# Kernel optimization log

Hardware: AMD Instinct MI355X
Metric: run time of the kernel (lower is better)

## Reference

```python
import jax, jax.numpy as jnp
import numpy as np

B, T, D, H = 4, 2048, 1024, 16
HD = D // H  # head_size = 64
EPS = 1e-5


def layernorm(x, g, b):
    mu = jnp.mean(x, axis=-1, keepdims=True)
    var = jnp.var(x, axis=-1, keepdims=True)
    return (x - mu) * jax.lax.rsqrt(var + EPS) * g + b


def setup_inputs() -> dict:
    key = jax.random.key(0)
    ks = jax.random.split(key, 8)
    s = 0.02
    return {
        "x": jax.random.normal(ks[0], (B, T, D), jnp.float32),
        "Wq": jax.random.normal(ks[1], (D, D), jnp.float32) * s,
        "Wk": jax.random.normal(ks[2], (D, D), jnp.float32) * s,
        "Wv": jax.random.normal(ks[3], (D, D), jnp.float32) * s,
        "Wo": jax.random.normal(ks[4], (D, D), jnp.float32) * s,
        "bo": jnp.zeros((D,), jnp.float32),
        "W1": jax.random.normal(ks[5], (D, 4 * D), jnp.float32) * s,
        "b1": jnp.zeros((4 * D,), jnp.float32),
        "W2": jax.random.normal(ks[6], (4 * D, D), jnp.float32) * s,
        "b2": jnp.zeros((D,), jnp.float32),
        "ln1_g": jnp.ones((D,), jnp.float32),
        "ln1_b": jnp.zeros((D,), jnp.float32),
        "ln2_g": jnp.ones((D,), jnp.float32),
        "ln2_b": jnp.zeros((D,), jnp.float32),
    }


def reference(x, Wq, Wk, Wv, Wo, bo, W1, b1, W2, b2, ln1_g, ln1_b, ln2_g, ln2_b):
    # --- multi-head causal self-attention (pre-LN), dropout off (eval) ---
    h = layernorm(x, ln1_g, ln1_b)
    q = jnp.einsum('btd,de->bte', h, Wq).reshape(B, T, H, HD)
    k = jnp.einsum('btd,de->bte', h, Wk).reshape(B, T, H, HD)
    v = jnp.einsum('btd,de->bte', h, Wv).reshape(B, T, H, HD)
    scores = jnp.einsum('bqhd,bkhd->bhqk', q, k) * (HD ** -0.5)
    causal = jnp.tril(jnp.ones((T, T), bool))
    scores = jnp.where(causal, scores, -jnp.inf)
    attn = jax.nn.softmax(scores, axis=-1)
    out = jnp.einsum('bhqk,bkhd->bqhd', attn, v).reshape(B, T, D)
    out = jnp.einsum('btd,de->bte', out, Wo) + bo
    x = x + out
    # --- feed-forward: Linear -> ReLU -> Linear -> ReLU (as in source) ---
    h2 = layernorm(x, ln2_g, ln2_b)
    ff = jax.nn.relu(jnp.einsum('btd,df->btf', h2, W1) + b1)
    ff = jax.nn.relu(jnp.einsum('btf,fd->btd', ff, W2) + b2)
    return x + ff
```

## Files before the change

### kernel.cpp

```cpp
#include <hip/hip_runtime.h>
#include <cstdint>
#include <cstddef>

typedef unsigned short u16;
typedef __attribute__((ext_vector_type(8))) short bf16x8;
typedef __attribute__((ext_vector_type(4))) float f32x4;
typedef __attribute__((address_space(1))) const unsigned int gu32;
typedef __attribute__((address_space(3))) unsigned int lu32;

#define QSCALE 0.1803368801111204f

__device__ __forceinline__ u16 f2bf(float f) {
  uint32_t u = __float_as_uint(f);
  u += 0x7fffu + ((u >> 16) & 1u);
  return (u16)(u >> 16);
}

__global__ __launch_bounds__(256) void transpose_w(const float* __restrict__ W,
                                                   u16* __restrict__ WT,
                                                   int K, int N) {
  __shared__ float t[32][33];
  int n0 = blockIdx.x * 32, k0 = blockIdx.y * 32;
  for (int i = threadIdx.y; i < 32; i += 8)
    t[i][threadIdx.x] = W[(size_t)(k0 + i) * N + n0 + threadIdx.x];
  __syncthreads();
  for (int i = threadIdx.y; i < 32; i += 8)
    WT[(size_t)(n0 + i) * K + k0 + threadIdx.x] = f2bf(t[threadIdx.x][i]);
}

__global__ __launch_bounds__(256) void ln_kernel(const float* __restrict__ x,
                                                 const float* __restrict__ g,
                                                 const float* __restrict__ b,
                                                 u16* __restrict__ out) {
  int row = blockIdx.x;
  const float4 v = *(const float4*)(x + (size_t)row * 1024 + threadIdx.x * 4);
  float s = v.x + v.y + v.z + v.w;
  float ss = v.x * v.x + v.y * v.y + v.z * v.z + v.w * v.w;
#pragma unroll
  for (int d = 1; d < 64; d <<= 1) { s += __shfl_xor(s, d); ss += __shfl_xor(ss, d); }
  __shared__ float rs_[4], rss_[4];
  int wv = threadIdx.x >> 6;
  if ((threadIdx.x & 63) == 0) { rs_[wv] = s; rss_[wv] = ss; }
  __syncthreads();
  s = rs_[0] + rs_[1] + rs_[2] + rs_[3];
  ss = rss_[0] + rss_[1] + rss_[2] + rss_[3];
  float mu = s * (1.f / 1024.f);
  float var = ss * (1.f / 1024.f) - mu * mu;
  float rstd = rsqrtf(var + 1e-5f);
  float4 gv = *(const float4*)(g + threadIdx.x * 4);
  float4 bv = *(const float4*)(b + threadIdx.x * 4);
  uint32_t lo = (uint32_t)f2bf((v.x - mu) * rstd * gv.x + bv.x) |
                ((uint32_t)f2bf((v.y - mu) * rstd * gv.y + bv.y) << 16);
  uint32_t hi = (uint32_t)f2bf((v.z - mu) * rstd * gv.z + bv.z) |
                ((uint32_t)f2bf((v.w - mu) * rstd * gv.w + bv.w) << 16);
  uint2 o; o.x = lo; o.y = hi;
  *(uint2*)(out + (size_t)row * 1024 + threadIdx.x * 4) = o;
}

#define STAGEA(slot, tnext, is)                                               \
  __builtin_amdgcn_global_load_lds(                                           \
      (gu32*)((const char*)(A + (size_t)(bm * 256 + (is) * 64 + srow) * K +   \
                            (size_t)(tnext) * 64) + ssw),                     \
      (lu32*)&lds[(slot) * 24576 + (is) * 4096 + wid * 512], 16, 0, 0)
#define STAGEB(slot, tnext, is)                                               \
  __builtin_amdgcn_global_load_lds(                                           \
      (gu32*)((const char*)(BT + (size_t)(bn * 128 + (is) * 64 + srow) * K +  \
                            (size_t)(tnext) * 64) + ssw),                     \
      (lu32*)&lds[(slot) * 24576 + 16384 + (is) * 4096 + wid * 512], 16, 0, 0)

template <int MODE>
__global__ __launch_bounds__(512, 2) void gemm8p(
    const u16* __restrict__ A, const u16* __restrict__ BT,
    int M, int N, int K,
    const float* __restrict__ bias, const float* __restrict__ resid,
    float* __restrict__ outf,
    u16* __restrict__ ob0, u16* __restrict__ ob1, u16* __restrict__ ob2) {
  __shared__ __align__(16) u16 lds[73728];
  const int tid = threadIdx.x, lane = tid & 63, wid = tid >> 6;
  const int wr = wid >> 1, wc = wid & 1;
  const int bm = blockIdx.y, bn = blockIdx.x;
  const int l15 = lane & 15, lhi = lane >> 4;
  const int srow = tid >> 3;
  const int ssw = ((tid & 7) * 16) ^ ((srow & 7) << 4);
  const int cs0 = (lhi * 8) ^ ((l15 & 7) << 3);
  const int cs1 = (32 + lhi * 8) ^ ((l15 & 7) << 3);
  const int arow = (wr * 64 + l15) * 64;
  const int brow = (wc * 64 + l15) * 64;

  f32x4 acc[4][4];
#pragma unroll
  for (int i = 0; i < 4; ++i)
#pragma unroll
    for (int j = 0; j < 4; ++j) acc[i][j] = (f32x4){0.f, 0.f, 0.f, 0.f};

  const int NT = K >> 6;

#pragma unroll
  for (int t0 = 0; t0 < 2; ++t0) {
    STAGEA(t0, t0, 0); STAGEA(t0, t0, 1); STAGEA(t0, t0, 2); STAGEA(t0, t0, 3);
    STAGEB(t0, t0, 0); STAGEB(t0, t0, 1);
  }
  asm volatile("s_waitcnt vmcnt(6)" ::: "memory");
  __builtin_amdgcn_s_barrier();

  int s = 0, sn = 2;
  for (int t = 0; t < NT; ++t) {
    const bool hasPre = (t + 2) < NT;
    const int aoff = s * 24576, boff = s * 24576 + 16384;

    bf16x8 bfr[4][2], afr[2][2];
#pragma unroll
    for (int ni = 0; ni < 4; ++ni) {
      bfr[ni][0] = *(const bf16x8*)&lds[boff + brow + ni * 1024 + cs0];
      bfr[ni][1] = *(const bf16x8*)&lds[boff + brow + ni * 1024 + cs1];
    }
    afr[0][0] = *(const bf16x8*)&lds[aoff + arow + cs0];
    afr[0][1] = *(const bf16x8*)&lds[aoff + arow + cs1];
    afr[1][0] = *(const bf16x8*)&lds[aoff + arow + 1024 + cs0];
    afr[1][1] = *(const bf16x8*)&lds[aoff + arow + 1024 + cs1];
    if (hasPre) { STAGEA(sn, t + 2, 0); STAGEA(sn, t + 2, 1); STAGEB(sn, t + 2, 0); }
    __builtin_amdgcn_s_barrier();
    __builtin_amdgcn_s_setprio(1);
#pragma unroll
    for (int ks = 0; ks < 2; ++ks)
#pragma unroll
      for (int ml = 0; ml < 2; ++ml)
#pragma unroll
        for (int ni = 0; ni < 4; ++ni)
          acc[ml][ni] = __builtin_amdgcn_mfma_f32_16x16x32_bf16(afr[ml][ks], bfr[ni][ks], acc[ml][ni], 0, 0, 0);
    __builtin_amdgcn_s_setprio(0);
    __builtin_amdgcn_s_barrier();

    afr[0][0] = *(const bf16x8*)&lds[aoff + arow + 2048 + cs0];
    afr[0][1] = *(const bf16x8*)&lds[aoff + arow + 2048 + cs1];
    afr[1][0] = *(const bf16x8*)&lds[aoff + arow + 3072 + cs0];
    afr[1][1] = *(const bf16x8*)&lds[aoff + arow + 3072 + cs1];
    if (hasPre) { STAGEA(sn, t + 2, 2); STAGEA(sn, t + 2, 3); STAGEB(sn, t + 2, 1); }
    __builtin_amdgcn_s_barrier();
    __builtin_amdgcn_s_setprio(1);
#pragma unroll
    for (int ks = 0; ks < 2; ++ks)
#pragma unroll
      for (int ml = 0; ml < 2; ++ml)
#pragma unroll
        for (int ni = 0; ni < 4; ++ni)
          acc[2 + ml][ni] = __builtin_amdgcn_mfma_f32_16x16x32_bf16(afr[ml][ks], bfr[ni][ks], acc[2 + ml][ni], 0, 0, 0);
    __builtin_amdgcn_s_setprio(0);
    if (hasPre) {
      asm volatile("s_waitcnt vmcnt(6)" ::: "memory");
    } else if (t + 1 < NT) {
      asm volatile("s_waitcnt vmcnt(0)" ::: "memory");
    }
    __builtin_amdgcn_s_barrier();

    s = (s == 2) ? 0 : s + 1;
    sn = (sn == 2) ? 0 : sn + 1;
  }

#pragma unroll
  for (int mi = 0; mi < 4; ++mi) {
#pragma unroll
    for (int ni = 0; ni < 4; ++ni) {
      int col = bn * 128 + wc * 64 + ni * 16 + l15;
      int rbase = bm * 256 + wr * 64 + mi * 16 + lhi * 4;
#pragma unroll
      for (int r = 0; r < 4; ++r) {
        float v = acc[mi][ni][r];
        int rg = rbase + r;
        if (MODE == 0) {
          int b = rg >> 11, tt = rg & 2047;
          int cm = col & 1023, h = cm >> 6, d = cm & 63;
          size_t bh = (size_t)(b * 16 + h);
          if (col < 1024)
            ob0[(bh * 2048 + tt) * 64 + d] = f2bf(v * QSCALE);
          else if (col < 2048)
            ob1[(bh * 2048 + tt) * 64 + d] = f2bf(v);
          else
            ob2[(bh * 64 + d) * 2048 + tt] = f2bf(v);
        } else if (MODE == 1) {
          outf[(size_t)rg * N + col] = v + bias[col] + resid[(size_t)rg * N + col];
        } else if (MODE == 2) {
          ob0[(size_t)rg * N + col] = f2bf(fmaxf(v + bias[col], 0.f));
        } else {
          outf[(size_t)rg * N + col] = fmaxf(v + bias[col], 0.f) + resid[(size_t)rg * N + col];
        }
      }
    }
  }
}

__global__ __launch_bounds__(512) void attn_kernel(
    const u16* __restrict__ Qb, const u16* __restrict__ Kb,
    const u16* __restrict__ VTb, u16* __restrict__ O) {
  const int p = blockIdx.x;
  const int bh = blockIdx.y;
  const u16* Q = Qb + (size_t)bh * 2048 * 64;
  const u16* Kp = Kb + (size_t)bh * 2048 * 64;
  const u16* VT = VTb + (size_t)bh * 64 * 2048;
  const int tid = threadIdx.x, lane = tid & 63, wv = tid >> 6;
  const int l15 = lane & 15, lhi = lane >> 4;
  const int srow = tid >> 3;
  const int scol16 = (tid & 7) * 16;
  const int sw = scol16 ^ ((srow & 7) << 4);
  const int rswz = (l15 & 7) << 4;
  const int cb0 = (lhi * 16) ^ rswz;
  const int cb1 = (64 + lhi * 16) ^ rswz;
  const int b = bh >> 4, h = bh & 15;

  __shared__ __align__(16) u16 KV[2][2][4096];
  __shared__ u16 Ps[8][16 * 72];

#define STAGEKV(slot, kt)                                                     \
  do {                                                                        \
    __builtin_amdgcn_global_load_lds(                                         \
        (gu32*)((const char*)(Kp + (size_t)((kt)*64 + srow) * 64) + sw),      \
        (lu32*)&KV[slot][0][wv * 512], 16, 0, 0);                             \
    __builtin_amdgcn_global_load_lds(                                         \
        (gu32*)((const char*)(VT + (size_t)srow * 2048 + (kt)*64) + sw),      \
        (lu32*)&KV[slot][1][wv * 512], 16, 0, 0);                             \
  } while (0)

#pragma unroll
  for (int pass = 0; pass < 2; ++pass) {
    const int chunk = pass ? p : (15 - p);
    const int qbase = chunk * 128 + wv * 16;
    const int nkt = 2 * chunk + 2;

    bf16x8 qf[2];
#pragma unroll
    for (int ks = 0; ks < 2; ++ks)
      qf[ks] = *(const bf16x8*)&Q[(size_t)(qbase + l15) * 64 + ks * 32 + lhi * 8];

    f32x4 o[4];
#pragma unroll
    for (int f = 0; f < 4; ++f) o[f] = (f32x4){0.f, 0.f, 0.f, 0.f};
    float m = -1e30f;
    float l = 0.f;

    __syncthreads();
    STAGEKV(0, 0);

    for (int kt = 0; kt < nkt; ++kt) {
      const int cs = kt & 1;
      asm volatile("s_waitcnt vmcnt(0)" ::: "memory");
      __syncthreads();
      if (kt + 1 < nkt) STAGEKV(cs ^ 1, kt + 1);

      if (kt * 64 <= qbase + 15) {
        const char* Kbase = (const char*)&KV[cs][0][0];
        const char* Vbase = (const char*)&KV[cs][1][0];

        f32x4 s[4];
#pragma unroll
        for (int jt = 0; jt < 4; ++jt) s[jt] = (f32x4){0.f, 0.f, 0.f, 0.f};
        __builtin_amdgcn_s_setprio(1);
#pragma unroll
        for (int ks = 0; ks < 2; ++ks) {
          const int cbyte = ks ? cb1 : cb0;
#pragma unroll
          for (int jt = 0; jt < 4; ++jt) {
            bf16x8 kf = *(const bf16x8*)(Kbase + (jt * 16 + l15) * 128 + cbyte);
            s[jt] = __builtin_amdgcn_mfma_f32_16x16x32_bf16(kf, qf[ks], s[jt], 0, 0, 0);
          }
        }
        __builtin_amdgcn_s_setprio(0);

        if (kt * 64 + 63 > qbase) {
          int qg = qbase + l15;
#pragma unroll
          for (int jt = 0; jt < 4; ++jt)
#pragma unroll
            for (int r = 0; r < 4; ++r) {
              int kg = kt * 64 + jt * 16 + lhi * 4 + r;
              if (kg > qg) s[jt][r] = -1e30f;
            }
        }

        float mr = fmaxf(fmaxf(s[0][0], s[0][1]), fmaxf(s[0][2], s[0][3]));
#pragma unroll
        for (int jt = 1; jt < 4; ++jt)
          mr = fmaxf(mr, fmaxf(fmaxf(s[jt][0], s[jt][1]), fmaxf(s[jt][2], s[jt][3])));
        mr = fmaxf(mr, __shfl_xor(mr, 16));
        mr = fmaxf(mr, __shfl_xor(mr, 32));
        if (__any(mr > m + 8.f)) {
          float mn = fmaxf(m, mr);
          float sc = exp2f(m - mn);
          l *= sc;
          m = mn;
#pragma unroll
          for (int r = 0; r < 4; ++r) {
            float so = __shfl(sc, lhi * 4 + r);
#pragma unroll
            for (int f = 0; f < 4; ++f) o[f][r] *= so;
          }
        }

        float rs = 0.f;
#pragma unroll
        for (int jt = 0; jt < 4; ++jt)
#pragma unroll
          for (int r = 0; r < 4; ++r) {
            float pv = exp2f(s[jt][r] - m);
            s[jt][r] = pv;
            rs += pv;
          }
        rs += __shfl_xor(rs, 16);
        rs += __shfl_xor(rs, 32);
        l += rs;

#pragma unroll
        for (int jt = 0; jt < 4; ++jt) {
          uint32_t lo, hi;
          asm("v_cvt_pk_bf16_f32 %0, %1, %2"
              : "=v"(lo) : "v"(s[jt][0]), "v"(s[jt][1]));
          asm("v_cvt_pk_bf16_f32 %0, %1, %2"
              : "=v"(hi) : "v"(s[jt][2]), "v"(s[jt][3]));
          uint2 pk; pk.x = lo; pk.y = hi;
          *(uint2*)&Ps[wv][l15 * 72 + jt * 16 + lhi * 4] = pk;
        }
        __builtin_amdgcn_s_setprio(1);
#pragma unroll
        for (int ks = 0; ks < 2; ++ks) {
          const int cbyte = ks ? cb1 : cb0;
          bf16x8 pf = *(const bf16x8*)&Ps[wv][l15 * 72 + ks * 32 + lhi * 8];
#pragma unroll
          for (int f = 0; f < 4; ++f) {
            bf16x8 vfr = *(const bf16x8*)(Vbase + (f * 16 + l15) * 128 + cbyte);
            o[f] = __builtin_amdgcn_mfma_f32_16x16x32_bf16(pf, vfr, o[f], 0, 0, 0);
          }
        }
        __builtin_amdgcn_s_setprio(0);
      }
    }

#pragma unroll
    for (int r = 0; r < 4; ++r) {
      float ld = __shfl(l, lhi * 4 + r);
      float inv = 1.f / ld;
      int t = qbase + lhi * 4 + r;
#pragma unroll
      for (int f = 0; f < 4; ++f)
        O[((size_t)(b * 2048 + t)) * 1024 + h * 64 + f * 16 + l15] = f2bf(o[f][r] * inv);
    }
  }
#undef STAGEKV
}

extern "C" void kernel_launch(void* const* d_in, const int* in_sizes, int n_in,
                              void* d_out, int out_size, void* d_ws, size_t ws_size,
                              hipStream_t stream) {
  const float* x   = (const float*)d_in[0];
  const float* Wq  = (const float*)d_in[1];
  const float* Wk  = (const float*)d_in[2];
  const float* Wv  = (const float*)d_in[3];
  const float* Wo  = (const float*)d_in[4];
  const float* bo  = (const float*)d_in[5];
  const float* W1  = (const float*)d_in[6];
  const float* b1  = (const float*)d_in[7];
  const float* W2  = (const float*)d_in[8];
  const float* b2  = (const float*)d_in[9];
  const float* g1  = (const float*)d_in[10];
  const float* be1 = (const float*)d_in[11];
  const float* g2  = (const float*)d_in[12];
  const float* be2 = (const float*)d_in[13];

  char* p = (char*)d_ws;
  auto alloc = [&](size_t bytes) {
    char* r = p;
    p += (bytes + 255) & ~(size_t)255;
    return r;
  };
  u16* WqkvT = (u16*)alloc(3072ull * 1024 * 2);
  u16* WoT   = (u16*)alloc(1024ull * 1024 * 2);
  u16* W1T   = (u16*)alloc(4096ull * 1024 * 2);
  u16* W2T   = (u16*)alloc(1024ull * 4096 * 2);
  u16* hln   = (u16*)alloc(8192ull * 1024 * 2);
  u16* Qbuf  = (u16*)alloc(8192ull * 1024 * 2);
  u16* Kbuf  = (u16*)alloc(8192ull * 1024 * 2);
  u16* VTbuf = (u16*)alloc(8192ull * 1024 * 2);
  float* x2  = (float*)alloc(8192ull * 1024 * 4);
  u16* ff1   = (u16*)alloc(8192ull * 4096 * 2);
  u16* Oattn = hln;
  u16* h2    = Qbuf;
  if ((size_t)(p - (char*)d_ws) > ws_size) return;

  dim3 tb(32, 8);
  transpose_w<<<dim3(32, 32), tb, 0, stream>>>(Wq, WqkvT, 1024, 1024);
  transpose_w<<<dim3(32, 32), tb, 0, stream>>>(Wk, WqkvT + 1024 * 1024, 1024, 1024);
  transpose_w<<<dim3(32, 32), tb, 0, stream>>>(Wv, WqkvT + 2048 * 1024, 1024, 1024);
  transpose_w<<<dim3(32, 32), tb, 0, stream>>>(Wo, WoT, 1024, 1024);
  transpose_w<<<dim3(128, 32), tb, 0, stream>>>(W1, W1T, 1024, 4096);
  transpose_w<<<dim3(32, 128), tb, 0, stream>>>(W2, W2T, 4096, 1024);

  ln_kernel<<<8192, 256, 0, stream>>>(x, g1, be1, hln);

  gemm8p<0><<<dim3(24, 32), 512, 0, stream>>>(hln, WqkvT, 8192, 3072, 1024,
                                              nullptr, nullptr, nullptr,
                                              Qbuf, Kbuf, VTbuf);

  attn_kernel<<<dim3(8, 64), 512, 0, stream>>>(Qbuf, Kbuf, VTbuf, Oattn);

  gemm8p<1><<<dim3(8, 32), 512, 0, stream>>>(Oattn, WoT, 8192, 1024, 1024,
                                             bo, x, x2, nullptr, nullptr, nullptr);

  ln_kernel<<<8192, 256, 0, stream>>>(x2, g2, be2, h2);

  gemm8p<2><<<dim3(32, 32), 512, 0, stream>>>(h2, W1T, 8192, 4096, 1024,
                                              b1, nullptr, nullptr, ff1, nullptr, nullptr);

  gemm8p<3><<<dim3(8, 32), 512, 0, stream>>>(ff1, W2T, 8192, 1024, 4096,
                                             b2, x2, (float*)d_out, nullptr, nullptr, nullptr);
}
```

Baseline: 432.2 us.

## Stage GEMM epilogue through LDS for coalesced vector stores; keep Q/K row-major

The bf16-output GEMM epilogues (QKV projection and FFN1) now write the converted accumulators into shared memory first, then emit 16-byte coalesced global stores. The V^T tile is transposed through LDS so stores run along the token dimension. Q and K are kept in plain [B,T,D] layout instead of a per-head layout, and the attention kernel reads them with a 1024-element row stride. This removes scattered 2-byte global stores in exchange for an extra LDS round trip and barrier. The attention kernel's K and Q loads become strided across heads.

New measurement: 403.9 us. 1.07x faster.

```diff
diff --git a/kernel.cpp b/kernel.cpp
--- a/kernel.cpp
+++ b/kernel.cpp
@@ -157,32 +157,88 @@
     sn = (sn == 2) ? 0 : sn + 1;
   }
 
-#pragma unroll
-  for (int mi = 0; mi < 4; ++mi) {
-#pragma unroll
-    for (int ni = 0; ni < 4; ++ni) {
-      int col = bn * 128 + wc * 64 + ni * 16 + l15;
-      int rbase = bm * 256 + wr * 64 + mi * 16 + lhi * 4;
-#pragma unroll
-      for (int r = 0; r < 4; ++r) {
-        float v = acc[mi][ni][r];
-        int rg = rbase + r;
-        if (MODE == 0) {
-          int b = rg >> 11, tt = rg & 2047;
-          int cm = col & 1023, h = cm >> 6, d = cm & 63;
-          size_t bh = (size_t)(b * 16 + h);
-          if (col < 1024)
-            ob0[(bh * 2048 + tt) * 64 + d] = f2bf(v * QSCALE);
-          else if (col < 2048)
-            ob1[(bh * 2048 + tt) * 64 + d] = f2bf(v);
+  if (MODE == 0 || MODE == 2) {
+    char* ep = (char*)lds;
+    const bool vmode = (MODE == 0) && (bn >= 16);
+    if (vmode) {
+#pragma unroll
+      for (int mi = 0; mi < 4; ++mi)
+#pragma unroll
+        for (int ni = 0; ni < 4; ++ni) {
+          uint32_t lo, hi;
+          asm("v_cvt_pk_bf16_f32 %0, %1, %2"
+              : "=v"(lo) : "v"(acc[mi][ni][0]), "v"(acc[mi][ni][1]));
+          asm("v_cvt_pk_bf16_f32 %0, %1, %2"
+              : "=v"(hi) : "v"(acc[mi][ni][2]), "v"(acc[mi][ni][3]));
+          uint2 pk; pk.x = lo; pk.y = hi;
+          int c_local = wc * 64 + ni * 16 + l15;
+          int rb = wr * 64 + mi * 16 + lhi * 4;
+          *(uint2*)(ep + c_local * 528 + rb * 2) = pk;
+        }
+    } else {
+      const float sc = (MODE == 0 && bn < 8) ? QSCALE : 1.f;
+#pragma unroll
+      for (int mi = 0; mi < 4; ++mi)
+#pragma unroll
+        for (int ni = 0; ni < 4; ++ni) {
+          int c_local = wc * 64 + ni * 16 + l15;
+          int rb = wr * 64 + mi * 16 + lhi * 4;
+          float bv = (MODE == 2) ? bias[bn * 128 + c_local] : 0.f;
+#pragma unroll
+          for (int r = 0; r < 4; ++r) {
+            float v = acc[mi][ni][r];
+            if (MODE == 2) v = fmaxf(v + bv, 0.f);
+            else v *= sc;
+            *(u16*)(ep + (rb + r) * 272 + c_local * 2) = f2bf(v);
+          }
+        }
+    }
+    __syncthreads();
+    if (vmode) {
+#pragma unroll
+      for (int i = 0; i < 8; ++i) {
+        int idx = i * 512 + tid;
+        int c = idx >> 5, tc = idx & 31;
+        uint4 d4 = *(const uint4*)(ep + c * 528 + tc * 16);
+        int cm = bn * 128 + c - 2048, hh = cm >> 6, dd = cm & 63;
+        size_t bh = (size_t)((bm >> 3) * 16 + hh);
+        int t0 = (bm & 7) * 256;
+        *(uint4*)&ob2[(bh * 64 + dd) * 2048 + t0 + tc * 8] = d4;
+      }
+    } else {
+#pragma unroll
+      for (int i = 0; i < 8; ++i) {
+        int idx = i * 512 + tid;
+        int row = idx >> 4, cc = idx & 15;
+        uint4 d4 = *(const uint4*)(ep + row * 272 + cc * 16);
+        size_t rg = (size_t)(bm * 256 + row);
+        if (MODE == 2) {
+          *(uint4*)&ob0[rg * N + bn * 128 + cc * 8] = d4;
+        } else {
+          int colg = bn * 128 + cc * 8;
+          if (colg < 1024)
+            *(uint4*)&ob0[rg * 1024 + colg] = d4;
           else
-            ob2[(bh * 64 + d) * 2048 + tt] = f2bf(v);
-        } else if (MODE == 1) {
-          outf[(size_t)rg * N + col] = v + bias[col] + resid[(size_t)rg * N + col];
-        } else if (MODE == 2) {
-          ob0[(size_t)rg * N + col] = f2bf(fmaxf(v + bias[col], 0.f));
-        } else {
-          outf[(size_t)rg * N + col] = fmaxf(v + bias[col], 0.f) + resid[(size_t)rg * N + col];
+            *(uint4*)&ob1[rg * 1024 + colg - 1024] = d4;
+        }
+      }
+    }
+  } else {
+#pragma unroll
+    for (int mi = 0; mi < 4; ++mi) {
+#pragma unroll
+      for (int ni = 0; ni < 4; ++ni) {
+        int col = bn * 128 + wc * 64 + ni * 16 + l15;
+        int rbase = bm * 256 + wr * 64 + mi * 16 + lhi * 4;
+#pragma unroll
+        for (int r = 0; r < 4; ++r) {
+          float v = acc[mi][ni][r];
+          int rg = rbase + r;
+          if (MODE == 1) {
+            outf[(size_t)rg * N + col] = v + bias[col] + resid[(size_t)rg * N + col];
+          } else {
+            outf[(size_t)rg * N + col] = fmaxf(v + bias[col], 0.f) + resid[(size_t)rg * N + col];
+          }
         }
       }
     }
@@ -194,8 +250,9 @@
     const u16* __restrict__ VTb, u16* __restrict__ O) {
   const int p = blockIdx.x;
   const int bh = blockIdx.y;
-  const u16* Q = Qb + (size_t)bh * 2048 * 64;
-  const u16* Kp = Kb + (size_t)bh * 2048 * 64;
+  const int b = bh >> 4, h = bh & 15;
+  const u16* Q = Qb + (size_t)b * 2048 * 1024 + h * 64;
+  const u16* Kn = Kb + (size_t)b * 2048 * 1024 + h * 64;
   const u16* VT = VTb + (size_t)bh * 64 * 2048;
   const int tid = threadIdx.x, lane = tid & 63, wv = tid >> 6;
   const int l15 = lane & 15, lhi = lane >> 4;
@@ -205,7 +262,6 @@
   const int rswz = (l15 & 7) << 4;
   const int cb0 = (lhi * 16) ^ rswz;
   const int cb1 = (64 + lhi * 16) ^ rswz;
-  const int b = bh >> 4, h = bh & 15;
 
   __shared__ __align__(16) u16 KV[2][2][4096];
   __shared__ u16 Ps[8][16 * 72];
@@ -213,7 +269,7 @@
 #define STAGEKV(slot, kt)                                                     \
   do {                                                                        \
     __builtin_amdgcn_global_load_lds(                                         \
-        (gu32*)((const char*)(Kp + (size_t)((kt)*64 + srow) * 64) + sw),      \
+        (gu32*)((const char*)(Kn + (size_t)((kt)*64 + srow) * 1024) + sw),    \
         (lu32*)&KV[slot][0][wv * 512], 16, 0, 0);                             \
     __builtin_amdgcn_global_load_lds(                                         \
         (gu32*)((const char*)(VT + (size_t)srow * 2048 + (kt)*64) + sw),      \
@@ -229,7 +285,7 @@
     bf16x8 qf[2];
 #pragma unroll
     for (int ks = 0; ks < 2; ++ks)
-      qf[ks] = *(const bf16x8*)&Q[(size_t)(qbase + l15) * 64 + ks * 32 + lhi * 8];
+      qf[ks] = *(const bf16x8*)&Q[(size_t)(qbase + l15) * 1024 + ks * 32 + lhi * 8];
 
     f32x4 o[4];
 #pragma unroll
```
